# Kernel tuning notes

Hardware: AMD Instinct MI355X
Metric: run time of the kernel (lower is better)

The kernel has to match this reference:

```python
import jax, jax.numpy as jnp
import numpy as np

HIDDEN = 1024
NUM_HEADS = 16
HEAD_DIM = HIDDEN // NUM_HEADS
ROPE_THETA = 10000.0


def rope_tables(seq_len, head_dim, theta):
    inv_freq = 1.0 / theta ** (jnp.arange(0, head_dim, 2, dtype=jnp.float32) / head_dim)
    pos = jnp.arange(seq_len, dtype=jnp.float32)
    freqs = jnp.outer(pos, inv_freq)  # [S, hd/2]
    return jnp.cos(freqs), jnp.sin(freqs)


def apply_rope(x, cos, sin):
    # x: [B, nh, S, hd]; cos/sin: [S, hd/2]
    x1, x2 = jnp.split(x, 2, axis=-1)
    return jnp.concatenate([x1 * cos - x2 * sin, x2 * cos + x1 * sin], axis=-1)


def setup_inputs() -> dict:
    key = jax.random.key(0)
    k1, k2, k3 = jax.random.split(key, 3)
    B, S = 2, 2048
    hidden_states = jax.random.normal(k1, (B, S, HIDDEN), dtype=jnp.float32)
    # nn.Linear stores weight as [out, in]; y = x @ W.T
    Wqkv = jax.random.normal(k2, (3 * HIDDEN, HIDDEN), dtype=jnp.float32) * (HIDDEN ** -0.5)
    Wo = jax.random.normal(k3, (HIDDEN, HIDDEN), dtype=jnp.float32) * (HIDDEN ** -0.5)
    return {"hidden_states": hidden_states, "Wqkv": Wqkv, "Wo": Wo}


def reference(hidden_states, Wqkv, Wo):
    B, S, H = hidden_states.shape
    qkv = hidden_states @ Wqkv.T  # [B, S, 3H]
    qkv = qkv.reshape(B, S, 3, NUM_HEADS, HEAD_DIM)
    q, k, v = jnp.moveaxis(qkv, 2, 0)  # each [B, S, nh, hd]
    q = jnp.transpose(q, (0, 2, 1, 3))  # [B, nh, S, hd]
    k = jnp.transpose(k, (0, 2, 1, 3))
    v = jnp.transpose(v, (0, 2, 1, 3))
    cos, sin = rope_tables(S, HEAD_DIM, ROPE_THETA)
    q = apply_rope(q, cos, sin)
    k = apply_rope(k, cos, sin)
    scale = 1.0 / jnp.sqrt(jnp.asarray(HEAD_DIM, dtype=q.dtype))
    scores = jnp.einsum("bhqd,bhkd->bhqk", q, k) * scale
    causal = jnp.tril(jnp.ones((S, S), dtype=bool))
    scores = jnp.where(causal, scores, jnp.finfo(scores.dtype).min)
    attn = jax.nn.softmax(scores, axis=-1)
    out = jnp.einsum("bhqk,bhkd->bhqd", attn, v)  # [B, nh, S, hd]
    out = jnp.transpose(out, (0, 2, 1, 3)).reshape(B, S, H)
    return out @ Wo.T
```

## Files before the change

### kernel.cpp

```cpp
#include <hip/hip_runtime.h>
#include <hip/hip_bf16.h>
#include <math.h>

typedef __bf16 bf16_t;
typedef __attribute__((ext_vector_type(8))) __bf16 bf16x8;
typedef __attribute__((ext_vector_type(4))) float f32x4;

#define AS1(p) ((__attribute__((address_space(1))) void*)(p))
#define AS3(p) ((__attribute__((address_space(3))) void*)(p))

__global__ void cvt_f32_bf16(const float* __restrict__ in, bf16_t* __restrict__ out, int n8) {
  int i = blockIdx.x * blockDim.x + threadIdx.x;
  if (i >= n8) return;
  const float4* p = (const float4*)in;
  float4 a = p[2 * i], b = p[2 * i + 1];
  bf16x8 o;
  o[0] = (bf16_t)a.x; o[1] = (bf16_t)a.y; o[2] = (bf16_t)a.z; o[3] = (bf16_t)a.w;
  o[4] = (bf16_t)b.x; o[5] = (bf16_t)b.y; o[6] = (bf16_t)b.z; o[7] = (bf16_t)b.w;
  ((bf16x8*)out)[i] = o;
}

__global__ void rope_tables_k(float* __restrict__ cosb, float* __restrict__ sinb) {
  int t = blockIdx.x * 256 + threadIdx.x;
  int s = t >> 5, i = t & 31;
  float inv = powf(10000.0f, -(float)i / 32.0f);
  float ang = (float)s * inv;
  float sv, cv;
  sincosf(ang, &sv, &cv);
  cosb[t] = cv;
  sinb[t] = sv;
}

__global__ __launch_bounds__(256)
void pack_rope(bf16_t* __restrict__ qkv, const float* __restrict__ cosb,
               const float* __restrict__ sinb, bf16_t* __restrict__ Kp) {
  __shared__ bf16_t vl[64][72];
  const int t = blockIdx.x, bh = blockIdx.y, b = bh >> 4, h = bh & 15;
  const int tid = threadIdx.x;
  const int r = tid >> 2, j = tid & 3;
  const int s = t * 64 + r;
  bf16_t* base = qkv + ((size_t)(b * 2048 + s)) * 3072 + h * 64;
  const float* cb = cosb + s * 32 + j * 8;
  const float* sb = sinb + s * 32 + j * 8;
  bf16x8 q1 = *(const bf16x8*)(base + j * 8);
  bf16x8 q2 = *(const bf16x8*)(base + j * 8 + 32);
  bf16x8 k1 = *(const bf16x8*)(base + 1024 + j * 8);
  bf16x8 k2 = *(const bf16x8*)(base + 1024 + j * 8 + 32);
  bf16x8 v1 = *(const bf16x8*)(base + 2048 + j * 8);
  bf16x8 v2 = *(const bf16x8*)(base + 2048 + j * 8 + 32);
  const float QS = 0.125f * 1.4426950408889634f;
  bf16x8 qo1, qo2, ko1, ko2;
#pragma unroll
  for (int i = 0; i < 8; ++i) {
    float c = cb[i], sn = sb[i];
    float a1 = (float)q1[i], a2 = (float)q2[i];
    qo1[i] = (bf16_t)((a1 * c - a2 * sn) * QS);
    qo2[i] = (bf16_t)((a2 * c + a1 * sn) * QS);
    float b1 = (float)k1[i], b2 = (float)k2[i];
    ko1[i] = (bf16_t)(b1 * c - b2 * sn);
    ko2[i] = (bf16_t)(b2 * c + b1 * sn);
  }
  *(bf16x8*)(base + j * 8) = qo1;
  *(bf16x8*)(base + j * 8 + 32) = qo2;
  bf16_t* kd = Kp + ((size_t)(bh * 32 + t)) * 4096 + r * 64;
  *(bf16x8*)(kd + ((j ^ (r & 7)) * 8)) = ko1;
  *(bf16x8*)(kd + (((j + 4) ^ (r & 7)) * 8)) = ko2;
#pragma unroll
  for (int i = 0; i < 8; ++i) { vl[r][j * 8 + i] = v1[i]; vl[r][j * 8 + 32 + i] = v2[i]; }
  __syncthreads();
  const int d = r;
  bf16x8 o1, o2;
#pragma unroll
  for (int i = 0; i < 8; ++i) { o1[i] = vl[j * 16 + i][d]; o2[i] = vl[j * 16 + 8 + i][d]; }
  bf16_t* vd = base + 2048;
  *(bf16x8*)(vd + (((2 * j) ^ (d & 7)) * 8)) = o1;
  *(bf16x8*)(vd + (((2 * j + 1) ^ (d & 7)) * 8)) = o2;
}

template <typename OutT>
__global__ __launch_bounds__(256, 2)
void gemm_nt(const bf16_t* __restrict__ A, const bf16_t* __restrict__ B,
             OutT* __restrict__ C, int M, int N, int K) {
  __shared__ __align__(16) bf16_t lA[128 * 64];
  __shared__ __align__(16) bf16_t lB[128 * 64];
  const int tid = threadIdx.x;
  const int wid = tid >> 6, lane = tid & 63;
  const int lr = lane & 15, lg = lane >> 4;
  const int nwg = gridDim.x * gridDim.y;
  int lin = blockIdx.y * gridDim.x + blockIdx.x;
  lin = (lin & 7) * (nwg >> 3) + (lin >> 3);
  const int m0 = (lin / gridDim.x) * 128, n0 = (lin % gridDim.x) * 128;
  const int wm = (wid >> 1) * 64, wn = (wid & 1) * 64;
  const int srow = lane >> 3;
  const int scol = (lane & 7) * 8;
  f32x4 acc[4][4];
#pragma unroll
  for (int i = 0; i < 4; ++i)
#pragma unroll
    for (int j = 0; j < 4; ++j) acc[i][j] = f32x4{0.f, 0.f, 0.f, 0.f};

  const int nk = K >> 6;
  for (int kt = 0; kt < nk; ++kt) {
    const int k0 = kt << 6;
    __syncthreads();
#pragma unroll
    for (int i = 0; i < 4; ++i) {
      int c = (wid << 2) + i;
      int r = (c << 3) + srow;
      __builtin_amdgcn_global_load_lds(AS1(A + (size_t)(m0 + r) * K + k0 + scol),
                                       AS3(&lA[c * 512]), 16, 0, 0);
      __builtin_amdgcn_global_load_lds(AS1(B + (size_t)(n0 + r) * K + k0 + scol),
                                       AS3(&lB[c * 512]), 16, 0, 0);
    }
    __syncthreads();
#pragma unroll
    for (int ks = 0; ks < 2; ++ks) {
      bf16x8 af[4], bfr[4];
#pragma unroll
      for (int i = 0; i < 4; ++i) {
        af[i]  = *(const bf16x8*)&lA[(wm + i * 16 + lr) * 64 + ks * 32 + lg * 8];
        bfr[i] = *(const bf16x8*)&lB[(wn + i * 16 + lr) * 64 + ks * 32 + lg * 8];
      }
#pragma unroll
      for (int i = 0; i < 4; ++i)
#pragma unroll
        for (int j = 0; j < 4; ++j)
          acc[i][j] = __builtin_amdgcn_mfma_f32_16x16x32_bf16(af[i], bfr[j], acc[i][j], 0, 0, 0);
    }
  }
#pragma unroll
  for (int i = 0; i < 4; ++i)
#pragma unroll
    for (int j = 0; j < 4; ++j)
#pragma unroll
      for (int r = 0; r < 4; ++r) {
        int row = m0 + wm + i * 16 + lg * 4 + r;
        int col = n0 + wn + j * 16 + lr;
        C[(size_t)row * N + col] = (OutT)acc[i][j][r];
      }
}

__global__ __launch_bounds__(256, 4)
void attn_fwd(const bf16_t* __restrict__ qkv, const bf16_t* __restrict__ Kp,
              bf16_t* __restrict__ O) {
  __shared__ __align__(16) bf16_t Ksh[2][4096];
  __shared__ __align__(16) bf16_t Vsh[2][4096];
  __shared__ __align__(16) bf16_t Psh[4][1024];
  const int tid = threadIdx.x, wid = tid >> 6, lane = tid & 63;
  const int lr = lane & 15, lg = lane >> 4;
  const int lin = blockIdx.y * 16 + blockIdx.x;
  const int c = (lin >> 3) & 15;
  const int bh = (lin & 7) | ((lin >> 7) << 3);
  const int b = bh >> 4, h = bh & 15;
  const int cA = c, cB = 31 - c;
  const int NI = 33;

  const bf16_t* QA = qkv + ((size_t)(b * 2048 + cA * 64 + wid * 16 + lr)) * 3072 + h * 64;
  const bf16_t* QB = qkv + ((size_t)(b * 2048 + cB * 64 + wid * 16 + lr)) * 3072 + h * 64;
  bf16x8 qA0 = *(const bf16x8*)(QA + lg * 8);
  bf16x8 qA1 = *(const bf16x8*)(QA + 32 + lg * 8);
  bf16x8 qB0 = *(const bf16x8*)(QB + lg * 8);
  bf16x8 qB1 = *(const bf16x8*)(QB + 32 + lg * 8);
  bf16x8 q0c = qA0, q1c = qA1;
  int qwc = cA * 64 + wid * 16;

  f32x4 o[4], oA[4];
  float lp[4], lpA[4];
#pragma unroll
  for (int r = 0; r < 4; ++r) { o[r] = f32x4{0.f, 0.f, 0.f, 0.f}; lp[r] = 0.f; }

  const int vr = tid >> 3, vc = tid & 7;
  const bf16_t* Kbase = Kp + ((size_t)bh * 32) * 4096 + tid * 8;
  const bf16_t* Vbase = qkv + ((size_t)(b * 2048 + vr)) * 3072 + 2048 + h * 64 + vc * 8;

#define TILE_OF(IT) ((IT) <= c ? (IT) : (IT) - (c + 1))
#define STAGE(IT, BUF)                                                                    \
  do {                                                                                    \
    int _t = TILE_OF(IT);                                                                 \
    __builtin_amdgcn_global_load_lds(AS1(Kbase + (size_t)_t * 4096),                      \
                                     AS3(&Ksh[BUF][tid * 8]), 16, 0, 0);                  \
    __builtin_amdgcn_global_load_lds(AS1(Kbase + (size_t)_t * 4096 + 2048),               \
                                     AS3(&Ksh[BUF][2048 + tid * 8]), 16, 0, 0);           \
    __builtin_amdgcn_global_load_lds(AS1(Vbase + (size_t)_t * 64 * 3072),                 \
                                     AS3(&Vsh[BUF][vr * 64 + vc * 8]), 16, 0, 0);         \
    __builtin_amdgcn_global_load_lds(AS1(Vbase + ((size_t)_t * 64 + 32) * 3072),          \
                                     AS3(&Vsh[BUF][(32 + vr) * 64 + vc * 8]), 16, 0, 0);  \
  } while (0)

  STAGE(0, 0);
  for (int i = 0; i < NI; ++i) {
    asm volatile("s_waitcnt vmcnt(0)" ::: "memory");
    __builtin_amdgcn_s_barrier();
    if (i + 1 < NI) STAGE(i + 1, (i + 1) & 1);
    const int buf = i & 1;
    const int k0 = TILE_OF(i) * 64;
    const bf16_t* K = &Ksh[buf][0];
    const bf16_t* V = &Vsh[buf][0];
    f32x4 s[4];
#pragma unroll
    for (int f = 0; f < 4; ++f) s[f] = f32x4{0.f, 0.f, 0.f, 0.f};
#pragma unroll
    for (int f = 0; f < 4; ++f) {
      int row = f * 16 + lr;
      bf16x8 kf0 = *(const bf16x8*)&K[row * 64 + ((lg ^ (row & 7)) * 8)];
      bf16x8 kf1 = *(const bf16x8*)&K[row * 64 + (((4 + lg) ^ (row & 7)) * 8)];
      s[f] = __builtin_amdgcn_mfma_f32_16x16x32_bf16(q0c, kf0, s[f], 0, 0, 0);
      s[f] = __builtin_amdgcn_mfma_f32_16x16x32_bf16(q1c, kf1, s[f], 0, 0, 0);
    }
    if (i == c || i == NI - 1) {
#pragma unroll
      for (int f = 0; f < 4; ++f)
#pragma unroll
        for (int r = 0; r < 4; ++r)
          if (k0 + f * 16 + lr > qwc + lg * 4 + r) s[f][r] = -3e38f;
    }
    bf16_t* P = &Psh[wid][0];
#pragma unroll
    for (int f = 0; f < 4; ++f)
#pragma unroll
      for (int r = 0; r < 4; ++r) {
        float pv = __builtin_amdgcn_exp2f(s[f][r]);
        lp[r] += pv;
        int q = lg * 4 + r;
        P[q * 64 + (((2 * f + (lr >> 3)) ^ (q & 7)) * 8) + (lr & 7)] = (bf16_t)pv;
      }
#pragma unroll
    for (int ks = 0; ks < 2; ++ks) {
      bf16x8 pa = *(const bf16x8*)&P[lr * 64 + (((ks * 4 + lg) ^ (lr & 7)) * 8)];
#pragma unroll
      for (int f2 = 0; f2 < 4; ++f2) {
        int row = f2 * 16 + lr;
        bf16x8 vb = *(const bf16x8*)&V[row * 64 + (((ks * 4 + lg) ^ (row & 7)) * 8)];
        o[f2] = __builtin_amdgcn_mfma_f32_16x16x32_bf16(pa, vb, o[f2], 0, 0, 0);
      }
    }
    if (i == c) {
#pragma unroll
      for (int r = 0; r < 4; ++r) {
        oA[r] = o[r]; lpA[r] = lp[r];
        o[r] = f32x4{0.f, 0.f, 0.f, 0.f}; lp[r] = 0.f;
      }
      q0c = qB0; q1c = qB1;
      qwc = cB * 64 + wid * 16;
    }
  }
#undef STAGE
#undef TILE_OF
  float invA[4], invB[4];
#pragma unroll
  for (int r = 0; r < 4; ++r) {
    float vB = lp[r], vA = lpA[r];
    vB += __shfl_xor(vB, 1, 64); vA += __shfl_xor(vA, 1, 64);
    vB += __shfl_xor(vB, 2, 64); vA += __shfl_xor(vA, 2, 64);
    vB += __shfl_xor(vB, 4, 64); vA += __shfl_xor(vA, 4, 64);
    vB += __shfl_xor(vB, 8, 64); vA += __shfl_xor(vA, 8, 64);
    invB[r] = 1.0f / vB; invA[r] = 1.0f / vA;
  }
#pragma unroll
  for (int f2 = 0; f2 < 4; ++f2)
#pragma unroll
    for (int r = 0; r < 4; ++r) {
      int d = f2 * 16 + lr;
      int qA_ = cA * 64 + wid * 16 + lg * 4 + r;
      int qB_ = cB * 64 + wid * 16 + lg * 4 + r;
      O[(((size_t)b * 2048 + qA_) * 16 + h) * 64 + d] = (bf16_t)(oA[f2][r] * invA[r]);
      O[(((size_t)b * 2048 + qB_) * 16 + h) * 64 + d] = (bf16_t)(o[f2][r] * invB[r]);
    }
}

extern "C" void kernel_launch(void* const* d_in, const int* in_sizes, int n_in,
                              void* d_out, int out_size, void* d_ws, size_t ws_size,
                              hipStream_t stream) {
  const float* hid  = (const float*)d_in[0];
  const float* wqkv = (const float*)d_in[1];
  const float* wo   = (const float*)d_in[2];
  float* out = (float*)d_out;
  char* ws = (char*)d_ws;
  bf16_t* hidb  = (bf16_t*)(ws);
  bf16_t* wqkvb = (bf16_t*)(ws + 8388608);
  bf16_t* wob   = (bf16_t*)(ws + 14680064);
  bf16_t* qkvb  = (bf16_t*)(ws + 16777216);
  float*  cosb  = (float*)(ws + 41943040);
  float*  sinb  = (float*)(ws + 42205184);
  bf16_t* Ob    = (bf16_t*)(ws + 42467328);
  bf16_t* Kp    = (bf16_t*)(ws);

  cvt_f32_bf16<<<2048, 256, 0, stream>>>(hid, hidb, 524288);
  cvt_f32_bf16<<<1536, 256, 0, stream>>>(wqkv, wqkvb, 393216);
  cvt_f32_bf16<<<512, 256, 0, stream>>>(wo, wob, 131072);
  rope_tables_k<<<256, 256, 0, stream>>>(cosb, sinb);
  gemm_nt<bf16_t><<<dim3(24, 32), 256, 0, stream>>>(hidb, wqkvb, qkvb, 4096, 3072, 1024);
  pack_rope<<<dim3(32, 32), 256, 0, stream>>>(qkvb, cosb, sinb, Kp);
  attn_fwd<<<dim3(16, 32), 256, 0, stream>>>(qkvb, Kp, Ob);
  gemm_nt<float><<<dim3(8, 32), 256, 0, stream>>>(Ob, wob, out, 4096, 1024, 1024);
}
```

Measured before the change: 125.2 us.

## Rewrite attention with 32x32 MFMA, register-resident P via permlane swap

The attention kernel now uses two waves of 32 query rows each, with 32x32x16 MFMA and transposed operands (K as A, Q as B), so that scores land in registers laid out for reuse. P no longer goes through shared memory: it is packed to bf16 and rearranged across lanes with v_permlane32_swap, then fed straight into the PV MFMA. The row-sum reduction is reduced to one shuffle, the first output half is written out early, and s_setprio brackets the MFMA sections. Blocks shrink to 128 threads with launch_bounds(128,1), which cuts waves per CU and so the latency hiding available. The wider 32x32 accumulators also raise register pressure.

```diff
diff --git a/kernel.cpp b/kernel.cpp
--- a/kernel.cpp
+++ b/kernel.cpp
@@ -5,6 +5,8 @@
 typedef __bf16 bf16_t;
 typedef __attribute__((ext_vector_type(8))) __bf16 bf16x8;
 typedef __attribute__((ext_vector_type(4))) float f32x4;
+typedef __attribute__((ext_vector_type(16))) float f32x16;
+typedef __attribute__((ext_vector_type(4))) unsigned u32x4;
 
 #define AS1(p) ((__attribute__((address_space(1))) void*)(p))
 #define AS3(p) ((__attribute__((address_space(3))) void*)(p))
@@ -140,51 +142,63 @@
       }
 }
 
-__global__ __launch_bounds__(256, 4)
+__device__ inline unsigned pkbf(float a, float b) {
+  bf16_t x = (bf16_t)a, y = (bf16_t)b;
+  return (unsigned)__builtin_bit_cast(unsigned short, x) |
+         ((unsigned)__builtin_bit_cast(unsigned short, y) << 16);
+}
+__device__ inline f32x16 zero16() {
+  f32x16 z;
+#pragma unroll
+  for (int r = 0; r < 16; ++r) z[r] = 0.f;
+  return z;
+}
+
+__global__ __launch_bounds__(128, 1)
 void attn_fwd(const bf16_t* __restrict__ qkv, const bf16_t* __restrict__ Kp,
               bf16_t* __restrict__ O) {
   __shared__ __align__(16) bf16_t Ksh[2][4096];
   __shared__ __align__(16) bf16_t Vsh[2][4096];
-  __shared__ __align__(16) bf16_t Psh[4][1024];
   const int tid = threadIdx.x, wid = tid >> 6, lane = tid & 63;
-  const int lr = lane & 15, lg = lane >> 4;
+  const int ln = lane & 31, h = lane >> 5;
   const int lin = blockIdx.y * 16 + blockIdx.x;
   const int c = (lin >> 3) & 15;
   const int bh = (lin & 7) | ((lin >> 7) << 3);
-  const int b = bh >> 4, h = bh & 15;
+  const int b = bh >> 4, hd = bh & 15;
   const int cA = c, cB = 31 - c;
   const int NI = 33;
 
-  const bf16_t* QA = qkv + ((size_t)(b * 2048 + cA * 64 + wid * 16 + lr)) * 3072 + h * 64;
-  const bf16_t* QB = qkv + ((size_t)(b * 2048 + cB * 64 + wid * 16 + lr)) * 3072 + h * 64;
-  bf16x8 qA0 = *(const bf16x8*)(QA + lg * 8);
-  bf16x8 qA1 = *(const bf16x8*)(QA + 32 + lg * 8);
-  bf16x8 qB0 = *(const bf16x8*)(QB + lg * 8);
-  bf16x8 qB1 = *(const bf16x8*)(QB + 32 + lg * 8);
-  bf16x8 q0c = qA0, q1c = qA1;
-  int qwc = cA * 64 + wid * 16;
-
-  f32x4 o[4], oA[4];
-  float lp[4], lpA[4];
-#pragma unroll
-  for (int r = 0; r < 4; ++r) { o[r] = f32x4{0.f, 0.f, 0.f, 0.f}; lp[r] = 0.f; }
-
-  const int vr = tid >> 3, vc = tid & 7;
+  const bf16_t* QArow = qkv + ((size_t)(b * 2048 + cA * 64 + wid * 32 + ln)) * 3072 + hd * 64;
+  const bf16_t* QBrow = qkv + ((size_t)(b * 2048 + cB * 64 + wid * 32 + ln)) * 3072 + hd * 64;
+  bf16x8 qA[4], qB[4], qc[4];
+#pragma unroll
+  for (int t = 0; t < 4; ++t) {
+    qA[t] = *(const bf16x8*)(QArow + t * 16 + h * 8);
+    qB[t] = *(const bf16x8*)(QBrow + t * 16 + h * 8);
+    qc[t] = qA[t];
+  }
+  int qwc = cA * 64 + wid * 32;
+
+  f32x16 o0 = zero16(), o1 = zero16();
+  float lp = 0.f;
+
   const bf16_t* Kbase = Kp + ((size_t)bh * 32) * 4096 + tid * 8;
-  const bf16_t* Vbase = qkv + ((size_t)(b * 2048 + vr)) * 3072 + 2048 + h * 64 + vc * 8;
+  const bf16_t* Vbase = qkv + ((size_t)(b * 2048 + (tid >> 3))) * 3072 + 2048 + hd * 64 + (tid & 7) * 8;
 
 #define TILE_OF(IT) ((IT) <= c ? (IT) : (IT) - (c + 1))
 #define STAGE(IT, BUF)                                                                    \
   do {                                                                                    \
     int _t = TILE_OF(IT);                                                                 \
-    __builtin_amdgcn_global_load_lds(AS1(Kbase + (size_t)_t * 4096),                      \
-                                     AS3(&Ksh[BUF][tid * 8]), 16, 0, 0);                  \
-    __builtin_amdgcn_global_load_lds(AS1(Kbase + (size_t)_t * 4096 + 2048),               \
-                                     AS3(&Ksh[BUF][2048 + tid * 8]), 16, 0, 0);           \
-    __builtin_amdgcn_global_load_lds(AS1(Vbase + (size_t)_t * 64 * 3072),                 \
-                                     AS3(&Vsh[BUF][vr * 64 + vc * 8]), 16, 0, 0);         \
-    __builtin_amdgcn_global_load_lds(AS1(Vbase + ((size_t)_t * 64 + 32) * 3072),          \
-                                     AS3(&Vsh[BUF][(32 + vr) * 64 + vc * 8]), 16, 0, 0);  \
+    const bf16_t* ks = Kbase + (size_t)_t * 4096;                                         \
+    __builtin_amdgcn_global_load_lds(AS1(ks),        AS3(&Ksh[BUF][tid * 8]), 16, 0, 0);  \
+    __builtin_amdgcn_global_load_lds(AS1(ks + 1024), AS3(&Ksh[BUF][1024 + tid * 8]), 16, 0, 0); \
+    __builtin_amdgcn_global_load_lds(AS1(ks + 2048), AS3(&Ksh[BUF][2048 + tid * 8]), 16, 0, 0); \
+    __builtin_amdgcn_global_load_lds(AS1(ks + 3072), AS3(&Ksh[BUF][3072 + tid * 8]), 16, 0, 0); \
+    const bf16_t* vs = Vbase + (size_t)_t * 64 * 3072;                                    \
+    __builtin_amdgcn_global_load_lds(AS1(vs),             AS3(&Vsh[BUF][tid * 8]), 16, 0, 0);        \
+    __builtin_amdgcn_global_load_lds(AS1(vs + 16 * 3072), AS3(&Vsh[BUF][1024 + tid * 8]), 16, 0, 0); \
+    __builtin_amdgcn_global_load_lds(AS1(vs + 32 * 3072), AS3(&Vsh[BUF][2048 + tid * 8]), 16, 0, 0); \
+    __builtin_amdgcn_global_load_lds(AS1(vs + 48 * 3072), AS3(&Vsh[BUF][3072 + tid * 8]), 16, 0, 0); \
   } while (0)
 
   STAGE(0, 0);
@@ -192,80 +206,93 @@
     asm volatile("s_waitcnt vmcnt(0)" ::: "memory");
     __builtin_amdgcn_s_barrier();
     if (i + 1 < NI) STAGE(i + 1, (i + 1) & 1);
-    const int buf = i & 1;
-    const int k0 = TILE_OF(i) * 64;
-    const bf16_t* K = &Ksh[buf][0];
-    const bf16_t* V = &Vsh[buf][0];
-    f32x4 s[4];
-#pragma unroll
-    for (int f = 0; f < 4; ++f) s[f] = f32x4{0.f, 0.f, 0.f, 0.f};
-#pragma unroll
-    for (int f = 0; f < 4; ++f) {
-      int row = f * 16 + lr;
-      bf16x8 kf0 = *(const bf16x8*)&K[row * 64 + ((lg ^ (row & 7)) * 8)];
-      bf16x8 kf1 = *(const bf16x8*)&K[row * 64 + (((4 + lg) ^ (row & 7)) * 8)];
-      s[f] = __builtin_amdgcn_mfma_f32_16x16x32_bf16(q0c, kf0, s[f], 0, 0, 0);
-      s[f] = __builtin_amdgcn_mfma_f32_16x16x32_bf16(q1c, kf1, s[f], 0, 0, 0);
-    }
+    const bf16_t* K = &Ksh[i & 1][0];
+    const bf16_t* V = &Vsh[i & 1][0];
+    f32x16 s0 = zero16(), s1 = zero16();
+    __builtin_amdgcn_s_setprio(1);
+#pragma unroll
+    for (int t = 0; t < 4; ++t) {
+      const int ch = 2 * t + h;
+      bf16x8 k0 = *(const bf16x8*)&K[ln * 64 + ((ch ^ (ln & 7)) * 8)];
+      bf16x8 k1 = *(const bf16x8*)&K[(32 + ln) * 64 + ((ch ^ (ln & 7)) * 8)];
+      s0 = __builtin_amdgcn_mfma_f32_32x32x16_bf16(k0, qc[t], s0, 0, 0, 0);
+      s1 = __builtin_amdgcn_mfma_f32_32x32x16_bf16(k1, qc[t], s1, 0, 0, 0);
+    }
+    __builtin_amdgcn_s_setprio(0);
     if (i == c || i == NI - 1) {
-#pragma unroll
-      for (int f = 0; f < 4; ++f)
-#pragma unroll
-        for (int r = 0; r < 4; ++r)
-          if (k0 + f * 16 + lr > qwc + lg * 4 + r) s[f][r] = -3e38f;
-    }
-    bf16_t* P = &Psh[wid][0];
-#pragma unroll
-    for (int f = 0; f < 4; ++f)
-#pragma unroll
-      for (int r = 0; r < 4; ++r) {
-        float pv = __builtin_amdgcn_exp2f(s[f][r]);
-        lp[r] += pv;
-        int q = lg * 4 + r;
-        P[q * 64 + (((2 * f + (lr >> 3)) ^ (q & 7)) * 8) + (lr & 7)] = (bf16_t)pv;
-      }
-#pragma unroll
-    for (int ks = 0; ks < 2; ++ks) {
-      bf16x8 pa = *(const bf16x8*)&P[lr * 64 + (((ks * 4 + lg) ^ (lr & 7)) * 8)];
-#pragma unroll
-      for (int f2 = 0; f2 < 4; ++f2) {
-        int row = f2 * 16 + lr;
-        bf16x8 vb = *(const bf16x8*)&V[row * 64 + (((ks * 4 + lg) ^ (row & 7)) * 8)];
-        o[f2] = __builtin_amdgcn_mfma_f32_16x16x32_bf16(pa, vb, o[f2], 0, 0, 0);
-      }
-    }
+      int qg = qwc + ln;
+      int k0g = TILE_OF(i) * 64;
+#pragma unroll
+      for (int r = 0; r < 16; ++r) {
+        int kv = k0g + (r & 3) + 8 * (r >> 2) + 4 * h;
+        if (kv > qg) s0[r] = -3e38f;
+        if (kv + 32 > qg) s1[r] = -3e38f;
+      }
+    }
+#pragma unroll
+    for (int r = 0; r < 16; ++r) {
+      float p0 = __builtin_amdgcn_exp2f(s0[r]); lp += p0; s0[r] = p0;
+      float p1 = __builtin_amdgcn_exp2f(s1[r]); lp += p1; s1[r] = p1;
+    }
+    __builtin_amdgcn_s_setprio(1);
+#pragma unroll
+    for (int t = 0; t < 4; ++t) {
+      const int u = t & 1;
+      f32x16 sv = (t >> 1) ? s1 : s0;
+      unsigned x  = pkbf(sv[8 * u + 0], sv[8 * u + 1]);
+      unsigned x2 = pkbf(sv[8 * u + 2], sv[8 * u + 3]);
+      unsigned y  = pkbf(sv[8 * u + 4], sv[8 * u + 5]);
+      unsigned y2 = pkbf(sv[8 * u + 6], sv[8 * u + 7]);
+      asm volatile("v_permlane32_swap_b32 %0, %1" : "+v"(x), "+v"(y));
+      asm volatile("v_permlane32_swap_b32 %0, %1" : "+v"(x2), "+v"(y2));
+      u32x4 pw; pw[0] = x; pw[1] = x2; pw[2] = y; pw[3] = y2;
+      bf16x8 pf = __builtin_bit_cast(bf16x8, pw);
+      const int ch = 2 * t + h;
+      bf16x8 v0 = *(const bf16x8*)&V[ln * 64 + ((ch ^ (ln & 7)) * 8)];
+      bf16x8 v1 = *(const bf16x8*)&V[(32 + ln) * 64 + ((ch ^ (ln & 7)) * 8)];
+      o0 = __builtin_amdgcn_mfma_f32_32x32x16_bf16(v0, pf, o0, 0, 0, 0);
+      o1 = __builtin_amdgcn_mfma_f32_32x32x16_bf16(v1, pf, o1, 0, 0, 0);
+    }
+    __builtin_amdgcn_s_setprio(0);
     if (i == c) {
-#pragma unroll
-      for (int r = 0; r < 4; ++r) {
-        oA[r] = o[r]; lpA[r] = lp[r];
-        o[r] = f32x4{0.f, 0.f, 0.f, 0.f}; lp[r] = 0.f;
-      }
-      q0c = qB0; q1c = qB1;
-      qwc = cB * 64 + wid * 16;
+      float lpf = lp + __shfl_xor(lp, 32, 64);
+      float inv = 1.0f / lpf;
+      bf16_t* Oaddr = O + ((size_t)(b * 2048 + qwc + ln)) * 1024 + hd * 64;
+#pragma unroll
+      for (int D = 0; D < 2; ++D) {
+        f32x16 ov = D ? o1 : o0;
+#pragma unroll
+        for (int Q = 0; Q < 4; ++Q) {
+          uint2 w;
+          w.x = pkbf(ov[4 * Q + 0] * inv, ov[4 * Q + 1] * inv);
+          w.y = pkbf(ov[4 * Q + 2] * inv, ov[4 * Q + 3] * inv);
+          *(uint2*)(Oaddr + D * 32 + Q * 8 + 4 * h) = w;
+        }
+      }
+      o0 = zero16(); o1 = zero16(); lp = 0.f;
+#pragma unroll
+      for (int t = 0; t < 4; ++t) qc[t] = qB[t];
+      qwc = cB * 64 + wid * 32;
     }
   }
 #undef STAGE
 #undef TILE_OF
-  float invA[4], invB[4];
-#pragma unroll
-  for (int r = 0; r < 4; ++r) {
-    float vB = lp[r], vA = lpA[r];
-    vB += __shfl_xor(vB, 1, 64); vA += __shfl_xor(vA, 1, 64);
-    vB += __shfl_xor(vB, 2, 64); vA += __shfl_xor(vA, 2, 64);
-    vB += __shfl_xor(vB, 4, 64); vA += __shfl_xor(vA, 4, 64);
-    vB += __shfl_xor(vB, 8, 64); vA += __shfl_xor(vA, 8, 64);
-    invB[r] = 1.0f / vB; invA[r] = 1.0f / vA;
-  }
-#pragma unroll
-  for (int f2 = 0; f2 < 4; ++f2)
-#pragma unroll
-    for (int r = 0; r < 4; ++r) {
-      int d = f2 * 16 + lr;
-      int qA_ = cA * 64 + wid * 16 + lg * 4 + r;
-      int qB_ = cB * 64 + wid * 16 + lg * 4 + r;
-      O[(((size_t)b * 2048 + qA_) * 16 + h) * 64 + d] = (bf16_t)(oA[f2][r] * invA[r]);
-      O[(((size_t)b * 2048 + qB_) * 16 + h) * 64 + d] = (bf16_t)(o[f2][r] * invB[r]);
-    }
+  {
+    float lpf = lp + __shfl_xor(lp, 32, 64);
+    float inv = 1.0f / lpf;
+    bf16_t* Oaddr = O + ((size_t)(b * 2048 + qwc + ln)) * 1024 + hd * 64;
+#pragma unroll
+    for (int D = 0; D < 2; ++D) {
+      f32x16 ov = D ? o1 : o0;
+#pragma unroll
+      for (int Q = 0; Q < 4; ++Q) {
+        uint2 w;
+        w.x = pkbf(ov[4 * Q + 0] * inv, ov[4 * Q + 1] * inv);
+        w.y = pkbf(ov[4 * Q + 2] * inv, ov[4 * Q + 3] * inv);
+        *(uint2*)(Oaddr + D * 32 + Q * 8 + 4 * h) = w;
+      }
+    }
+  }
 }
 
 extern "C" void kernel_launch(void* const* d_in, const int* in_sizes, int n_in,
@@ -291,6 +318,6 @@
   rope_tables_k<<<256, 256, 0, stream>>>(cosb, sinb);
   gemm_nt<bf16_t><<<dim3(24, 32), 256, 0, stream>>>(hidb, wqkvb, qkvb, 4096, 3072, 1024);
   pack_rope<<<dim3(32, 32), 256, 0, stream>>>(qkvb, cosb, sinb, Kp);
-  attn_fwd<<<dim3(16, 32), 256, 0, stream>>>(qkvb, Kp, Ob);
+  attn_fwd<<<dim3(16, 32), 128, 0, stream>>>(qkvb, Kp, Ob);
   gemm_nt<float><<<dim3(8, 32), 256, 0, stream>>>(Ob, wob, out, 4096, 1024, 1024);
 }
```

Result: slower. 140.2 us (+12.0%).
